# Optimization experiments

Hardware: AMD Instinct MI355X
Metric: run time of the kernel (lower is better)

## Reference

```python
import jax, jax.numpy as jnp
import numpy as np

B, T, C, H = 2, 2048, 768, 12
HD = C // H  # head dim = 64
EPS = 1e-5


def layer_norm(x, g, b):
    mu = jnp.mean(x, axis=-1, keepdims=True)
    var = jnp.var(x, axis=-1, keepdims=True)
    return (x - mu) * jax.lax.rsqrt(var + EPS) * g + b


def setup_inputs() -> dict:
    key = jax.random.key(0)
    ks = jax.random.split(key, 5)
    s = 0.02
    return {
        "x": jax.random.normal(ks[0], (B, T, C), jnp.float32),
        "ln1_g": jnp.ones((C,), jnp.float32),
        "ln1_b": jnp.zeros((C,), jnp.float32),
        "W_qkv": jax.random.normal(ks[1], (C, 3 * C), jnp.float32) * s,
        "W_attn_proj": jax.random.normal(ks[2], (C, C), jnp.float32) * s,
        "ln2_g": jnp.ones((C,), jnp.float32),
        "ln2_b": jnp.zeros((C,), jnp.float32),
        "W_fc": jax.random.normal(ks[3], (C, 4 * C), jnp.float32) * s,
        "W_mlp_proj": jax.random.normal(ks[4], (4 * C, C), jnp.float32) * s,
    }


def attention(x, W_qkv, W_attn_proj):
    b, t, c = x.shape
    qkv = x @ W_qkv  # [B,T,3C]
    q, k, v = jnp.split(qkv, 3, axis=-1)
    # [B,H,T,HD]
    q = q.reshape(b, t, H, HD).transpose(0, 2, 1, 3)
    k = k.reshape(b, t, H, HD).transpose(0, 2, 1, 3)
    v = v.reshape(b, t, H, HD).transpose(0, 2, 1, 3)
    att = jnp.einsum("bhqd,bhkd->bhqk", q, k) * (1.0 / np.sqrt(HD).astype(np.float32))
    causal = jnp.tril(jnp.ones((t, t), jnp.bool_))
    att = jnp.where(causal, att, jnp.finfo(att.dtype).min)
    att = jax.nn.softmax(att, axis=-1)
    y = jnp.einsum("bhqk,bhkd->bhqd", att, v)
    y = y.transpose(0, 2, 1, 3).reshape(b, t, c)
    return y @ W_attn_proj


def mlp(x, W_fc, W_mlp_proj):
    h = jax.nn.gelu(x @ W_fc, approximate=False)
    return h @ W_mlp_proj


def reference(x, ln1_g, ln1_b, W_qkv, W_attn_proj, ln2_g, ln2_b, W_fc, W_mlp_proj):
    x = x + attention(layer_norm(x, ln1_g, ln1_b), W_qkv, W_attn_proj)
    x = x + mlp(layer_norm(x, ln2_g, ln2_b), W_fc, W_mlp_proj)
    return x
```

## Files before the change

### kernel.cpp

```cpp
#include <hip/hip_runtime.h>
#include <cstdint>
#include <cstddef>

typedef unsigned short u16;
typedef __attribute__((ext_vector_type(4))) float f32x4;
typedef __attribute__((ext_vector_type(8))) short bf16x8;

__device__ __forceinline__ u16 f2bf(float f) {
  unsigned int u = __builtin_bit_cast(unsigned int, f);
  u += 0x7fffu + ((u >> 16) & 1u);
  return (u16)(u >> 16);
}

__device__ __forceinline__ void gl_lds16(const u16* g, u16* lds_base) {
  __builtin_amdgcn_global_load_lds(
      (const __attribute__((address_space(1))) unsigned int*)g,
      (__attribute__((address_space(3))) unsigned int*)lds_base, 16, 0, 0);
}

__global__ __launch_bounds__(256) void transpose_all(const float* __restrict__ s0,
                                                     const float* __restrict__ s1,
                                                     const float* __restrict__ s2,
                                                     const float* __restrict__ s3,
                                                     u16* __restrict__ d0,
                                                     u16* __restrict__ d1,
                                                     u16* __restrict__ d2,
                                                     u16* __restrict__ d3) {
  __shared__ float tile[32][33];
  int idx = blockIdx.x;
  const float* src; u16* dst; int K, N, t;
  if (idx < 1728)      { src = s0; dst = d0; K = 768;  N = 2304; t = idx; }
  else if (idx < 2304) { src = s1; dst = d1; K = 768;  N = 768;  t = idx - 1728; }
  else if (idx < 4608) { src = s2; dst = d2; K = 768;  N = 3072; t = idx - 2304; }
  else                 { src = s3; dst = d3; K = 3072; N = 768;  t = idx - 4608; }
  int nt_n = N >> 5;
  int n0 = (t % nt_n) * 32, k0 = (t / nt_n) * 32;
  int tx = threadIdx.x & 31, ty = threadIdx.x >> 5;
#pragma unroll
  for (int i = 0; i < 4; ++i)
    tile[ty + i * 8][tx] = src[(size_t)(k0 + ty + i * 8) * N + n0 + tx];
  __syncthreads();
#pragma unroll
  for (int i = 0; i < 4; ++i)
    dst[(size_t)(n0 + ty + i * 8) * K + k0 + tx] = f2bf(tile[tx][ty + i * 8]);
}

__global__ __launch_bounds__(256) void transpose_v(const u16* __restrict__ qkvb,
                                                   u16* __restrict__ vt,
                                                   unsigned int* __restrict__ ctr) {
  __shared__ u16 tile[64 * 72];
  if (blockIdx.x == 0 && blockIdx.y == 0 && threadIdx.x == 0) *ctr = 0u;
  int t0 = blockIdx.x * 64;
  int bh = blockIdx.y;
  int b = bh / 12, h = bh % 12;
  int tid = threadIdx.x;
  int c8 = tid & 7, r = tid >> 3;
#pragma unroll
  for (int i = 0; i < 2; ++i) {
    int rr = r + i * 32;
    *(uint4*)&tile[rr * 72 + c8 * 8] =
        *(const uint4*)&qkvb[(size_t)(b * 2048 + t0 + rr) * 2304 + 1536 + h * 64 + c8 * 8];
  }
  __syncthreads();
#pragma unroll
  for (int i = 0; i < 2; ++i) {
    int dr = r + i * 32;
    u16 tmp[8];
#pragma unroll
    for (int j = 0; j < 8; ++j) tmp[j] = tile[(c8 * 8 + j) * 72 + dr];
    *(uint4*)&vt[((size_t)bh * 64 + dr) * 2048 + t0 + c8 * 8] = *(uint4*)tmp;
  }
}

__global__ __launch_bounds__(192) void ln_rows(const float* __restrict__ x,
                                               const float* __restrict__ g,
                                               const float* __restrict__ bb,
                                               u16* __restrict__ out) {
  int row = blockIdx.x;
  int t = threadIdx.x;
  float4 v = *(const float4*)(x + (size_t)row * 768 + t * 4);
  float s = v.x + v.y + v.z + v.w;
  float sq = v.x * v.x + v.y * v.y + v.z * v.z + v.w * v.w;
#pragma unroll
  for (int o = 32; o > 0; o >>= 1) {
    s += __shfl_down(s, o);
    sq += __shfl_down(sq, o);
  }
  __shared__ float ss[3], s2[3];
  int w = t >> 6;
  if ((t & 63) == 0) { ss[w] = s; s2[w] = sq; }
  __syncthreads();
  s = ss[0] + ss[1] + ss[2];
  sq = s2[0] + s2[1] + s2[2];
  float mu = s * (1.f / 768.f);
  float var = sq * (1.f / 768.f) - mu * mu;
  float rs = rsqrtf(var + 1e-5f);
  float4 gv = *(const float4*)(g + t * 4);
  float4 bv = *(const float4*)(bb + t * 4);
  u16 o4[4];
  o4[0] = f2bf((v.x - mu) * rs * gv.x + bv.x);
  o4[1] = f2bf((v.y - mu) * rs * gv.y + bv.y);
  o4[2] = f2bf((v.z - mu) * rs * gv.z + bv.z);
  o4[3] = f2bf((v.w - mu) * rs * gv.w + bv.w);
  *(uint2*)(out + (size_t)row * 768 + t * 4) = *(uint2*)o4;
}

template <int EPI, int TM>
__global__ __launch_bounds__(256, 3) void gemm_bt(const u16* __restrict__ A,
                                                  const u16* __restrict__ BT,
                                                  int M, int N, int K,
                                                  float* __restrict__ outF,
                                                  u16* __restrict__ outB,
                                                  const float* __restrict__ res) {
  constexpr int MT = TM / 64;
  __shared__ __align__(16) u16 Al[2][TM * 64];
  __shared__ __align__(16) u16 Bl[2][64 * 64];
  int tid = threadIdx.x;
  int lane = tid & 63, w = tid >> 6;
  int l16 = lane & 15, quad = lane >> 4;
  int swz = l16 & 7;
  size_t rowA0 = (size_t)blockIdx.y * TM;
  size_t rowB0 = (size_t)blockIdx.x * 64;

  auto stage = [&](int buf, int k0) {
#pragma unroll
    for (int i = 0; i < TM / 32; ++i) {
      int cbase = (i * 4 + w) * 64;
      int chunk = cbase + lane;
      int r = chunk >> 3, c8 = (chunk & 7) ^ (r & 7);
      gl_lds16(&A[(rowA0 + r) * (size_t)K + k0 + c8 * 8], &Al[buf][cbase * 8]);
    }
#pragma unroll
    for (int i = 0; i < 2; ++i) {
      int cbase = (i * 4 + w) * 64;
      int chunk = cbase + lane;
      int r = chunk >> 3, c8 = (chunk & 7) ^ (r & 7);
      gl_lds16(&BT[(rowB0 + r) * (size_t)K + k0 + c8 * 8], &Bl[buf][cbase * 8]);
    }
  };

  f32x4 acc[MT][4] = {};
  stage(0, 0);
  int cur = 0;
  for (int k0 = 0; k0 < K; k0 += 64) {
    __syncthreads();
    if (k0 + 64 < K) stage(cur ^ 1, k0 + 64);
#pragma unroll
    for (int ks = 0; ks < 2; ++ks) {
      int c = ks * 4 + quad;
      bf16x8 af[MT], bf[4];
#pragma unroll
      for (int mt = 0; mt < MT; ++mt)
        af[mt] = *(const bf16x8*)&Al[cur][(w * (TM / 4) + mt * 16 + l16) * 64 + (c ^ swz) * 8];
#pragma unroll
      for (int nt = 0; nt < 4; ++nt)
        bf[nt] = *(const bf16x8*)&Bl[cur][(nt * 16 + l16) * 64 + (c ^ swz) * 8];
#pragma unroll
      for (int mt = 0; mt < MT; ++mt)
#pragma unroll
        for (int nt = 0; nt < 4; ++nt)
          acc[mt][nt] = __builtin_amdgcn_mfma_f32_16x16x32_bf16(af[mt], bf[nt], acc[mt][nt], 0, 0, 0);
    }
    cur ^= 1;
  }

#pragma unroll
  for (int mt = 0; mt < MT; ++mt) {
#pragma unroll
    for (int i = 0; i < 4; ++i) {
      size_t row = rowA0 + w * (TM / 4) + mt * 16 + quad * 4 + i;
#pragma unroll
      for (int nt = 0; nt < 4; ++nt) {
        size_t col = rowB0 + nt * 16 + l16;
        float v = acc[mt][nt][i];
        if (EPI == 0) {
          outB[row * N + col] = f2bf(v);
        } else if (EPI == 1) {
          outF[row * N + col] = res[row * N + col] + v;
        } else {
          float ge = 0.5f * v * (1.f + erff(v * 0.70710678118654752f));
          outB[row * N + col] = f2bf(ge);
        }
      }
    }
  }
}

__global__ __launch_bounds__(256, 3) void flash_attn(const u16* __restrict__ qkv,
                                                     const u16* __restrict__ vt,
                                                     u16* __restrict__ y,
                                                     unsigned int* __restrict__ ctr) {
  __shared__ __align__(16) u16 Kl[128 * 64];
  __shared__ __align__(16) u16 Vl[64 * 128];
  __shared__ __align__(16) u16 Pl[4][16 * 136];
  __shared__ unsigned int s_unit;

  int tid = threadIdx.x;
  int lane = tid & 63, w = tid >> 6;
  int l16 = lane & 15, quad = lane >> 4;
  int swz = l16 & 7;
  u16* Pw = &Pl[w][0];

  for (;;) {
    __syncthreads();
    if (tid == 0) s_unit = atomicAdd(ctr, 1u);
    __syncthreads();
    unsigned int u = s_unit;
    if (u >= 768u) return;

    int qt = 31 - (int)(u / 24u);
    int bh = (int)(u % 24u);
    int b = bh / 12, h = bh % 12;
    int qw = qt * 64 + w * 16;

    const u16* base = qkv + (size_t)b * 2048 * 2304;
    const u16* vbase = vt + (size_t)bh * 64 * 2048;

    bf16x8 qf0, qf1;
    {
      const u16* qp = base + (size_t)(qw + l16) * 2304 + h * 64 + quad * 8;
      qf0 = *(const bf16x8*)qp;
      qf1 = *(const bf16x8*)(qp + 32);
    }

    f32x4 O[4] = {};
    float l_i[4] = {0.f, 0.f, 0.f, 0.f};

    int nkb = qt / 2 + 1;
    const float sc = 0.125f * 1.44269504088896340736f;
    for (int kb = 0; kb < nkb; ++kb) {
      int kt0 = kb << 7;
      __syncthreads();
#pragma unroll
      for (int i = 0; i < 4; ++i) {
        int cbase = (i * 4 + w) * 64;
        int chunk = cbase + lane;
        int r = chunk >> 3, c8 = (chunk & 7) ^ (r & 7);
        gl_lds16(base + (size_t)(kt0 + r) * 2304 + 768 + h * 64 + c8 * 8, &Kl[cbase * 8]);
      }
#pragma unroll
      for (int i = 0; i < 4; ++i) {
        int cbase = (i * 4 + w) * 64;
        int chunk = cbase + lane;
        int r = chunk >> 4, c16 = (chunk & 15) ^ (r & 7);
        gl_lds16(vbase + (size_t)r * 2048 + kt0 + c16 * 8, &Vl[cbase * 8]);
      }
      __syncthreads();

      f32x4 S[8];
#pragma unroll
      for (int nt = 0; nt < 8; ++nt) {
        bf16x8 k0 = *(const bf16x8*)&Kl[(nt * 16 + l16) * 64 + (quad ^ swz) * 8];
        bf16x8 k1 = *(const bf16x8*)&Kl[(nt * 16 + l16) * 64 + ((4 + quad) ^ swz) * 8];
        f32x4 z = {};
        z = __builtin_amdgcn_mfma_f32_16x16x32_bf16(qf0, k0, z, 0, 0, 0);
        S[nt] = __builtin_amdgcn_mfma_f32_16x16x32_bf16(qf1, k1, z, 0, 0, 0);
      }

      bool diag = (kb == nkb - 1);
#pragma unroll
      for (int nt = 0; nt < 8; ++nt) {
        int tk = kt0 + nt * 16 + l16;
#pragma unroll
        for (int i = 0; i < 4; ++i) {
          float p = exp2f(S[nt][i] * sc);
          if (diag && tk > qw + quad * 4 + i) p = 0.f;
          l_i[i] += p;
          Pw[(quad * 4 + i) * 136 + nt * 16 + l16] =
              (u16)(__builtin_bit_cast(unsigned int, p) >> 16);
        }
      }

      asm volatile("s_waitcnt lgkmcnt(0)" ::: "memory");

#pragma unroll
      for (int c = 0; c < 4; ++c) {
        bf16x8 pf = *(const bf16x8*)&Pw[l16 * 136 + c * 32 + quad * 8];
#pragma unroll
        for (int dt = 0; dt < 4; ++dt) {
          bf16x8 vf = *(const bf16x8*)&Vl[(dt * 16 + l16) * 128 + ((c * 4 + quad) ^ swz) * 8];
          O[dt] = __builtin_amdgcn_mfma_f32_16x16x32_bf16(pf, vf, O[dt], 0, 0, 0);
        }
      }
    }

#pragma unroll
    for (int i = 0; i < 4; ++i) {
#pragma unroll
      for (int o = 1; o < 16; o <<= 1) l_i[i] += __shfl_xor(l_i[i], o);
    }
#pragma unroll
    for (int dt = 0; dt < 4; ++dt) {
#pragma unroll
      for (int i = 0; i < 4; ++i) {
        int tq = qw + quad * 4 + i;
        float ov = O[dt][i] / l_i[i];
        y[(size_t)(b * 2048 + tq) * 768 + h * 64 + dt * 16 + l16] = f2bf(ov);
      }
    }
  }
}

extern "C" void kernel_launch(void* const* d_in, const int* in_sizes, int n_in,
                              void* d_out, int out_size, void* d_ws, size_t ws_size,
                              hipStream_t stream) {
  const float* x      = (const float*)d_in[0];
  const float* ln1_g  = (const float*)d_in[1];
  const float* ln1_b  = (const float*)d_in[2];
  const float* W_qkv  = (const float*)d_in[3];
  const float* W_attn = (const float*)d_in[4];
  const float* ln2_g  = (const float*)d_in[5];
  const float* ln2_b  = (const float*)d_in[6];
  const float* W_fc   = (const float*)d_in[7];
  const float* W_mlp  = (const float*)d_in[8];
  float* out = (float*)d_out;

  const int M = 4096;
  char* p = (char*)d_ws;
  auto alloc = [&](size_t bytes) {
    char* r = p;
    p += (bytes + 255) & ~(size_t)255;
    return r;
  };
  u16* wt_qkv  = (u16*)alloc((size_t)2304 * 768 * 2);
  u16* wt_attn = (u16*)alloc((size_t)768 * 768 * 2);
  u16* wt_fc   = (u16*)alloc((size_t)3072 * 768 * 2);
  u16* wt_mlp  = (u16*)alloc((size_t)768 * 3072 * 2);
  u16* xn1     = (u16*)alloc((size_t)M * 768 * 2);
  u16* qkvb    = (u16*)alloc((size_t)M * 2304 * 2);
  u16* yb      = (u16*)alloc((size_t)M * 768 * 2);
  float* x1    = (float*)alloc((size_t)M * 768 * 4);
  u16* xn2     = (u16*)alloc((size_t)M * 768 * 2);
  u16* hb      = (u16*)alloc((size_t)M * 3072 * 2);
  u16* vt      = (u16*)alloc((size_t)24 * 64 * 2048 * 2);
  unsigned int* ctr = (unsigned int*)alloc(256);

  transpose_all<<<6912, 256, 0, stream>>>(W_qkv, W_attn, W_fc, W_mlp,
                                          wt_qkv, wt_attn, wt_fc, wt_mlp);

  ln_rows<<<M, 192, 0, stream>>>(x, ln1_g, ln1_b, xn1);
  gemm_bt<0, 128><<<dim3(2304 / 64, M / 128), 256, 0, stream>>>(xn1, wt_qkv, M, 2304, 768,
                                                                nullptr, qkvb, nullptr);
  transpose_v<<<dim3(32, 24), 256, 0, stream>>>(qkvb, vt, ctr);
  flash_attn<<<768, 256, 0, stream>>>(qkvb, vt, yb, ctr);
  gemm_bt<1, 64><<<dim3(768 / 64, M / 64), 256, 0, stream>>>(yb, wt_attn, M, 768, 768,
                                                             x1, nullptr, x);
  ln_rows<<<M, 192, 0, stream>>>(x1, ln2_g, ln2_b, xn2);
  gemm_bt<2, 128><<<dim3(3072 / 64, M / 128), 256, 0, stream>>>(xn2, wt_fc, M, 3072, 768,
                                                                nullptr, hb, nullptr);
  gemm_bt<1, 64><<<dim3(768 / 64, M / 64), 256, 0, stream>>>(hb, wt_mlp, M, 768, 3072,
                                                             out, nullptr, x1);
}
```

Measured before the change: 273.5 us.

## Use 128x128 GEMM tiles and double-buffered 64-key K/V staging in attention

Adds a GEMM configuration with 128x128 output tiles, where the four waves are arranged 2x2 and each computes a 64x64 sub-tile; it is applied to the QKV and FC projections to raise operand reuse per LDS load. Flash attention switches from single-buffered 128-key blocks to double-buffered 64-key blocks, prefetching the next K/V tile while the current one computes and dropping the post-load barrier. The trade-offs are higher register pressure (occupancy hint lowered to 2) and fewer GEMM blocks per wave of CUs. The attention loop now runs twice as many iterations.

```diff
diff --git a/kernel.cpp b/kernel.cpp
--- a/kernel.cpp
+++ b/kernel.cpp
@@ -105,22 +105,25 @@
   *(uint2*)(out + (size_t)row * 768 + t * 4) = *(uint2*)o4;
 }
 
-template <int EPI, int TM>
-__global__ __launch_bounds__(256, 3) void gemm_bt(const u16* __restrict__ A,
-                                                  const u16* __restrict__ BT,
-                                                  int M, int N, int K,
-                                                  float* __restrict__ outF,
-                                                  u16* __restrict__ outB,
-                                                  const float* __restrict__ res) {
-  constexpr int MT = TM / 64;
+template <int EPI, int CFG>
+__global__ __launch_bounds__(256, (CFG == 0) ? 2 : 3)
+void gemm_bt(const u16* __restrict__ A, const u16* __restrict__ BT,
+             int M, int N, int K,
+             float* __restrict__ outF, u16* __restrict__ outB,
+             const float* __restrict__ res) {
+  constexpr int TM = (CFG == 0) ? 128 : 64;
+  constexpr int TN = (CFG == 0) ? 128 : 64;
+  constexpr int MT = (CFG == 0) ? 4 : 1;
   __shared__ __align__(16) u16 Al[2][TM * 64];
-  __shared__ __align__(16) u16 Bl[2][64 * 64];
+  __shared__ __align__(16) u16 Bl[2][TN * 64];
   int tid = threadIdx.x;
   int lane = tid & 63, w = tid >> 6;
   int l16 = lane & 15, quad = lane >> 4;
   int swz = l16 & 7;
+  int wrow = (CFG == 0) ? (w >> 1) * 64 : w * 16;
+  int wcol = (CFG == 0) ? (w & 1) * 64 : 0;
   size_t rowA0 = (size_t)blockIdx.y * TM;
-  size_t rowB0 = (size_t)blockIdx.x * 64;
+  size_t rowB0 = (size_t)blockIdx.x * TN;
 
   auto stage = [&](int buf, int k0) {
 #pragma unroll
@@ -131,7 +134,7 @@
       gl_lds16(&A[(rowA0 + r) * (size_t)K + k0 + c8 * 8], &Al[buf][cbase * 8]);
     }
 #pragma unroll
-    for (int i = 0; i < 2; ++i) {
+    for (int i = 0; i < TN / 32; ++i) {
       int cbase = (i * 4 + w) * 64;
       int chunk = cbase + lane;
       int r = chunk >> 3, c8 = (chunk & 7) ^ (r & 7);
@@ -151,10 +154,10 @@
       bf16x8 af[MT], bf[4];
 #pragma unroll
       for (int mt = 0; mt < MT; ++mt)
-        af[mt] = *(const bf16x8*)&Al[cur][(w * (TM / 4) + mt * 16 + l16) * 64 + (c ^ swz) * 8];
+        af[mt] = *(const bf16x8*)&Al[cur][(wrow + mt * 16 + l16) * 64 + (c ^ swz) * 8];
 #pragma unroll
       for (int nt = 0; nt < 4; ++nt)
-        bf[nt] = *(const bf16x8*)&Bl[cur][(nt * 16 + l16) * 64 + (c ^ swz) * 8];
+        bf[nt] = *(const bf16x8*)&Bl[cur][(wcol + nt * 16 + l16) * 64 + (c ^ swz) * 8];
 #pragma unroll
       for (int mt = 0; mt < MT; ++mt)
 #pragma unroll
@@ -168,10 +171,10 @@
   for (int mt = 0; mt < MT; ++mt) {
 #pragma unroll
     for (int i = 0; i < 4; ++i) {
-      size_t row = rowA0 + w * (TM / 4) + mt * 16 + quad * 4 + i;
+      size_t row = rowA0 + wrow + mt * 16 + quad * 4 + i;
 #pragma unroll
       for (int nt = 0; nt < 4; ++nt) {
-        size_t col = rowB0 + nt * 16 + l16;
+        size_t col = rowB0 + wcol + nt * 16 + l16;
         float v = acc[mt][nt][i];
         if (EPI == 0) {
           outB[row * N + col] = f2bf(v);
@@ -190,9 +193,9 @@
                                                      const u16* __restrict__ vt,
                                                      u16* __restrict__ y,
                                                      unsigned int* __restrict__ ctr) {
-  __shared__ __align__(16) u16 Kl[128 * 64];
-  __shared__ __align__(16) u16 Vl[64 * 128];
-  __shared__ __align__(16) u16 Pl[4][16 * 136];
+  __shared__ __align__(16) u16 Kl[2][64 * 64];
+  __shared__ __align__(16) u16 Vl[2][64 * 64];
+  __shared__ __align__(16) u16 Pl[4][16 * 72];
   __shared__ unsigned int s_unit;
 
   int tid = threadIdx.x;
@@ -200,6 +203,7 @@
   int l16 = lane & 15, quad = lane >> 4;
   int swz = l16 & 7;
   u16* Pw = &Pl[w][0];
+  const float sc = 0.125f * 1.44269504088896340736f;
 
   for (;;) {
     __syncthreads();
@@ -216,6 +220,23 @@
     const u16* base = qkv + (size_t)b * 2048 * 2304;
     const u16* vbase = vt + (size_t)bh * 64 * 2048;
 
+    auto stage = [&](int buf, int t0) {
+#pragma unroll
+      for (int i = 0; i < 2; ++i) {
+        int cbase = (i * 4 + w) * 64;
+        int chunk = cbase + lane;
+        int r = chunk >> 3, c8 = (chunk & 7) ^ (r & 7);
+        gl_lds16(base + (size_t)(t0 + r) * 2304 + 768 + h * 64 + c8 * 8, &Kl[buf][cbase * 8]);
+      }
+#pragma unroll
+      for (int i = 0; i < 2; ++i) {
+        int cbase = (i * 4 + w) * 64;
+        int chunk = cbase + lane;
+        int r = chunk >> 3, c8 = (chunk & 7) ^ (r & 7);
+        gl_lds16(vbase + (size_t)r * 2048 + t0 + c8 * 8, &Vl[buf][cbase * 8]);
+      }
+    };
+
     bf16x8 qf0, qf1;
     {
       const u16* qp = base + (size_t)(qw + l16) * 2304 + h * 64 + quad * 8;
@@ -226,32 +247,19 @@
     f32x4 O[4] = {};
     float l_i[4] = {0.f, 0.f, 0.f, 0.f};
 
-    int nkb = qt / 2 + 1;
-    const float sc = 0.125f * 1.44269504088896340736f;
+    int nkb = qt + 1;
+    stage(0, 0);
+    int cur = 0;
     for (int kb = 0; kb < nkb; ++kb) {
-      int kt0 = kb << 7;
+      int kt0 = kb << 6;
       __syncthreads();
-#pragma unroll
-      for (int i = 0; i < 4; ++i) {
-        int cbase = (i * 4 + w) * 64;
-        int chunk = cbase + lane;
-        int r = chunk >> 3, c8 = (chunk & 7) ^ (r & 7);
-        gl_lds16(base + (size_t)(kt0 + r) * 2304 + 768 + h * 64 + c8 * 8, &Kl[cbase * 8]);
-      }
-#pragma unroll
-      for (int i = 0; i < 4; ++i) {
-        int cbase = (i * 4 + w) * 64;
-        int chunk = cbase + lane;
-        int r = chunk >> 4, c16 = (chunk & 15) ^ (r & 7);
-        gl_lds16(vbase + (size_t)r * 2048 + kt0 + c16 * 8, &Vl[cbase * 8]);
-      }
-      __syncthreads();
-
-      f32x4 S[8];
-#pragma unroll
-      for (int nt = 0; nt < 8; ++nt) {
-        bf16x8 k0 = *(const bf16x8*)&Kl[(nt * 16 + l16) * 64 + (quad ^ swz) * 8];
-        bf16x8 k1 = *(const bf16x8*)&Kl[(nt * 16 + l16) * 64 + ((4 + quad) ^ swz) * 8];
+      if (kb + 1 < nkb) stage(cur ^ 1, kt0 + 64);
+
+      f32x4 S[4];
+#pragma unroll
+      for (int nt = 0; nt < 4; ++nt) {
+        bf16x8 k0 = *(const bf16x8*)&Kl[cur][(nt * 16 + l16) * 64 + (quad ^ swz) * 8];
+        bf16x8 k1 = *(const bf16x8*)&Kl[cur][(nt * 16 + l16) * 64 + ((4 + quad) ^ swz) * 8];
         f32x4 z = {};
         z = __builtin_amdgcn_mfma_f32_16x16x32_bf16(qf0, k0, z, 0, 0, 0);
         S[nt] = __builtin_amdgcn_mfma_f32_16x16x32_bf16(qf1, k1, z, 0, 0, 0);
@@ -259,14 +267,14 @@
 
       bool diag = (kb == nkb - 1);
 #pragma unroll
-      for (int nt = 0; nt < 8; ++nt) {
+      for (int nt = 0; nt < 4; ++nt) {
         int tk = kt0 + nt * 16 + l16;
 #pragma unroll
         for (int i = 0; i < 4; ++i) {
           float p = exp2f(S[nt][i] * sc);
           if (diag && tk > qw + quad * 4 + i) p = 0.f;
           l_i[i] += p;
-          Pw[(quad * 4 + i) * 136 + nt * 16 + l16] =
+          Pw[(quad * 4 + i) * 72 + nt * 16 + l16] =
               (u16)(__builtin_bit_cast(unsigned int, p) >> 16);
         }
       }
@@ -274,14 +282,15 @@
       asm volatile("s_waitcnt lgkmcnt(0)" ::: "memory");
 
 #pragma unroll
-      for (int c = 0; c < 4; ++c) {
-        bf16x8 pf = *(const bf16x8*)&Pw[l16 * 136 + c * 32 + quad * 8];
+      for (int c = 0; c < 2; ++c) {
+        bf16x8 pf = *(const bf16x8*)&Pw[l16 * 72 + c * 32 + quad * 8];
 #pragma unroll
         for (int dt = 0; dt < 4; ++dt) {
-          bf16x8 vf = *(const bf16x8*)&Vl[(dt * 16 + l16) * 128 + ((c * 4 + quad) ^ swz) * 8];
+          bf16x8 vf = *(const bf16x8*)&Vl[cur][(dt * 16 + l16) * 64 + ((c * 4 + quad) ^ swz) * 8];
           O[dt] = __builtin_amdgcn_mfma_f32_16x16x32_bf16(pf, vf, O[dt], 0, 0, 0);
         }
       }
+      cur ^= 1;
     }
 
 #pragma unroll
@@ -339,15 +348,15 @@
                                           wt_qkv, wt_attn, wt_fc, wt_mlp);
 
   ln_rows<<<M, 192, 0, stream>>>(x, ln1_g, ln1_b, xn1);
-  gemm_bt<0, 128><<<dim3(2304 / 64, M / 128), 256, 0, stream>>>(xn1, wt_qkv, M, 2304, 768,
-                                                                nullptr, qkvb, nullptr);
+  gemm_bt<0, 0><<<dim3(2304 / 128, M / 128), 256, 0, stream>>>(xn1, wt_qkv, M, 2304, 768,
+                                                               nullptr, qkvb, nullptr);
   transpose_v<<<dim3(32, 24), 256, 0, stream>>>(qkvb, vt, ctr);
   flash_attn<<<768, 256, 0, stream>>>(qkvb, vt, yb, ctr);
-  gemm_bt<1, 64><<<dim3(768 / 64, M / 64), 256, 0, stream>>>(yb, wt_attn, M, 768, 768,
-                                                             x1, nullptr, x);
+  gemm_bt<1, 1><<<dim3(768 / 64, M / 64), 256, 0, stream>>>(yb, wt_attn, M, 768, 768,
+                                                            x1, nullptr, x);
   ln_rows<<<M, 192, 0, stream>>>(x1, ln2_g, ln2_b, xn2);
-  gemm_bt<2, 128><<<dim3(3072 / 64, M / 128), 256, 0, stream>>>(xn2, wt_fc, M, 3072, 768,
-                                                                nullptr, hb, nullptr);
-  gemm_bt<1, 64><<<dim3(768 / 64, M / 64), 256, 0, stream>>>(hb, wt_mlp, M, 768, 3072,
-                                                             out, nullptr, x1);
-}
+  gemm_bt<2, 0><<<dim3(3072 / 128, M / 128), 256, 0, stream>>>(xn2, wt_fc, M, 3072, 768,
+                                                               nullptr, hb, nullptr);
+  gemm_bt<1, 1><<<dim3(768 / 64, M / 64), 256, 0, stream>>>(hb, wt_mlp, M, 768, 3072,
+                                                            out, nullptr, x1);
+}
```

Result: slower. 284.6 us (+4.1%).
